# Performance work log

Hardware: AMD Instinct MI355X
Metric: run time of the kernel (lower is better)

Reference implementation:

```python
import jax, jax.numpy as jnp
import numpy as np

D = 128        # node/time feature dim (n_node_features)
E = 20         # edge feature dim (hard-coded in TGS)
N = 4096       # number of source nodes
K = 10         # neighbors per node (hard-coded n_neighbors=10)
NUM_NODES = 100000
NUM_EDGES = 500000


def setup_inputs() -> dict:
    key = jax.random.key(0)
    ks = jax.random.split(key, 11)
    node_features = jax.random.normal(ks[0], (NUM_NODES, D), jnp.float32)
    edge_features = jax.random.normal(ks[1], (NUM_EDGES, E), jnp.float32)
    source_nodes = jax.random.randint(ks[2], (N,), 0, NUM_NODES)
    timestamps = jax.random.uniform(ks[3], (N,), jnp.float32) * 1000.0
    neighbors1 = jax.random.randint(ks[4], (N, K), 0, NUM_NODES)
    edge_idxs1 = jax.random.randint(ks[5], (N, K), 0, NUM_EDGES)
    edge_times1 = jax.random.uniform(ks[6], (N, K), jnp.float32) * 1000.0
    neighbors2 = jax.random.randint(ks[7], (N * K, K), 0, NUM_NODES)
    edge_idxs2 = jax.random.randint(ks[8], (N * K, K), 0, NUM_EDGES)
    edge_times2 = jax.random.uniform(ks[9], (N * K, K), jnp.float32) * 1000.0
    # TimeEncode params (TGN init: w = 1/10^linspace(0,9,D), b = 0)
    time_w = jnp.asarray(1.0 / 10.0 ** np.linspace(0, 9, D), jnp.float32)
    time_b = jnp.zeros((D,), jnp.float32)
    pk = jax.random.split(ks[10], 4)
    s1 = float(1.0 / np.sqrt(2 * D + E))
    lin1_w = jax.random.uniform(pk[0], (2, 2 * D + E, D), jnp.float32, -s1, s1)
    lin1_b = jax.random.uniform(pk[1], (2, D), jnp.float32, -s1, s1)
    s2 = float(1.0 / np.sqrt(3 * D))
    lin2_w = jax.random.uniform(pk[2], (2, 3 * D, D), jnp.float32, -s2, s2)
    lin2_b = jax.random.uniform(pk[3], (2, D), jnp.float32, -s2, s2)
    return dict(node_features=node_features, edge_features=edge_features,
                source_nodes=source_nodes, timestamps=timestamps,
                neighbors1=neighbors1, edge_idxs1=edge_idxs1, edge_times1=edge_times1,
                neighbors2=neighbors2, edge_idxs2=edge_idxs2, edge_times2=edge_times2,
                time_w=time_w, time_b=time_b,
                lin1_w=lin1_w, lin1_b=lin1_b, lin2_w=lin2_w, lin2_b=lin2_b)


def reference(node_features, edge_features, source_nodes, timestamps,
              neighbors1, edge_idxs1, edge_times1,
              neighbors2, edge_idxs2, edge_times2,
              time_w, time_b, lin1_w, lin1_b, lin2_w, lin2_b):
    def time_enc(t):
        # TGN TimeEncode: cos(t * w + b), broadcast over feature dim
        return jnp.cos(t[..., None] * time_w + time_b)

    def aggregate(layer, src_feat, src_time_emb, nbr_emb, edge_time_emb, edge_feat):
        # GraphSumEmbedding.aggregate
        nf = jnp.concatenate([nbr_emb, edge_time_emb, edge_feat], axis=-1)  # [n, K, 2D+E]
        h = nf @ lin1_w[layer] + lin1_b[layer]                              # [n, K, D]
        nbr_sum = jax.nn.relu(h.sum(axis=1))                                # [n, D]
        sf = jnp.concatenate([src_feat, src_time_emb, nbr_sum], axis=-1)   # [n, 3D]
        return sf @ lin2_w[layer] + lin2_b[layer]                           # [n, D]

    n, k = neighbors1.shape
    ts1 = jnp.repeat(timestamps, k)  # timestamps for the N*K first-hop neighbors

    # recursion level 1 (layer index 0): embed the N*K first-hop neighbors;
    # their neighbors' (level-0) embeddings are raw node features.
    emb1 = aggregate(
        0,
        node_features[neighbors1.reshape(-1)],          # [N*K, D]
        time_enc(jnp.zeros_like(ts1)),                  # [N*K, D]
        node_features[neighbors2],                      # [N*K, K, D]
        time_enc(ts1[:, None] - edge_times2),           # [N*K, K, D]
        edge_features[edge_idxs2])                      # [N*K, K, E]

    # recursion level 2 (layer index 1): embed the N source nodes
    emb2 = aggregate(
        1,
        node_features[source_nodes],                    # [N, D]
        time_enc(jnp.zeros_like(timestamps)),           # [N, D]
        emb1.reshape(n, k, -1),                         # [N, K, D]
        time_enc(timestamps[:, None] - edge_times1),    # [N, K, D]
        edge_features[edge_idxs1])                      # [N, K, E]
    return emb2
```

## Files before the change

kernel.cpp:

```cpp
#include <hip/hip_runtime.h>

#define TGS_D 128
#define TGS_E 20
#define TGS_K 10
#define TGS_F1 276
#define LDA1 296
#define LDA2 264
#define RPB 16

typedef _Float16 f16;
typedef _Float16 f16x4 __attribute__((ext_vector_type(4)));
typedef _Float16 f16x8 __attribute__((ext_vector_type(8)));
typedef float    f32x4 __attribute__((ext_vector_type(4)));

__global__ void tgs_pack_w1(const float* __restrict__ W1, f16x8* __restrict__ PW1) {
    const int b = blockIdx.x, lane = threadIdx.x;
    const int layer = b / 72, rem = b % 72, ntile = rem / 9, kk = rem % 9;
    const int colg = ntile * 16 + (lane & 15);
    const int kbase = kk * 32 + (lane >> 4) * 8;
    f16x8 v;
    #pragma unroll
    for (int j = 0; j < 8; ++j) {
        const int k = kbase + j;
        v[j] = (k < TGS_F1) ? (f16)W1[(layer * TGS_F1 + k) * TGS_D + colg] : (f16)0.f;
    }
    PW1[b * 64 + lane] = v;
}

__global__ void tgs_pack_w2(const float* __restrict__ W2, f16x8* __restrict__ PW2) {
    const int b = blockIdx.x, lane = threadIdx.x;
    const int layer = b / 64, rem = b % 64, ntile = rem / 8, kk = rem % 8;
    const int colg = ntile * 16 + (lane & 15);
    const int kbase = kk * 32 + (lane >> 4) * 8;
    f16x8 v;
    #pragma unroll
    for (int j = 0; j < 8; ++j) {
        const int k = kbase + j;
        const int w2row = (k < TGS_D) ? k : (k + TGS_D);
        v[j] = (f16)W2[(layer * 3 * TGS_D + w2row) * TGS_D + colg];
    }
    PW2[b * 64 + lane] = v;
}

__global__ __launch_bounds__(128)
void tgs_tvec_kernel(const float* __restrict__ tb, const float* __restrict__ W2,
                     const float* __restrict__ B2, float* __restrict__ tvec) {
    const int l = blockIdx.x, d = threadIdx.x;
    const float* w = W2 + (l * 3 * TGS_D + TGS_D) * TGS_D;
    float acc = B2[l * TGS_D + d];
    for (int j = 0; j < TGS_D; ++j)
        acc = fmaf(__cosf(tb[j]), w[j * TGS_D + d], acc);
    tvec[l * TGS_D + d] = acc;
}

template<int LEVEL>
__global__ __launch_bounds__(256, 6)
void tgs_agg_kernel(
    const float* __restrict__ NF, const float* __restrict__ EF,
    const int* __restrict__ src_ids, const float* __restrict__ ts_arr,
    const int* __restrict__ nbr_idx,
    const int* __restrict__ eidx, const float* __restrict__ etime,
    const float* __restrict__ emb_in,
    const float* __restrict__ tw, const float* __restrict__ tb,
    const f16x8* __restrict__ PW1, const float* __restrict__ B1,
    const f16x8* __restrict__ PW2, const float* __restrict__ tvec,
    float* __restrict__ out)
{
    __shared__ f16 snf[RPB][LDA1];
    __shared__ f16 sf2[RPB][LDA2];
    __shared__ int   s_nbr[RPB * TGS_K];
    __shared__ int   s_eid[RPB * TGS_K];
    __shared__ float s_et [RPB * TGS_K];
    __shared__ float s_ts [RPB];

    const int tid = threadIdx.x;
    const int base_row = blockIdx.x * RPB;

    if (tid < RPB * TGS_K) {
        if (LEVEL == 1) s_nbr[tid] = nbr_idx[base_row * TGS_K + tid];
        s_eid[tid] = eidx[base_row * TGS_K + tid];
        s_et [tid] = etime[base_row * TGS_K + tid];
    }
    if (tid < RPB)
        s_ts[tid] = (LEVEL == 1) ? ts_arr[(base_row + tid) / TGS_K] : ts_arr[base_row + tid];
    __syncthreads();

    {
        const int sub = tid & 31;
        const int rr  = tid >> 5;
        const float4 wv = ((const float4*)tw)[sub];
        const float4 bv = ((const float4*)tb)[sub];
        #pragma unroll
        for (int h = 0; h < 2; ++h) {
            const int r   = h * 8 + rr;
            const int row = base_row + r;

            float4 a = make_float4(0.f, 0.f, 0.f, 0.f);
            if (LEVEL == 1) {
                #pragma unroll
                for (int k = 0; k < TGS_K; ++k) {
                    const int nb = s_nbr[r * TGS_K + k];
                    const float4 v = ((const float4*)(NF + nb * TGS_D))[sub];
                    a.x += v.x; a.y += v.y; a.z += v.z; a.w += v.w;
                }
            } else {
                #pragma unroll
                for (int k = 0; k < TGS_K; ++k) {
                    const float4 v = ((const float4*)(emb_in + (row * TGS_K + k) * TGS_D))[sub];
                    a.x += v.x; a.y += v.y; a.z += v.z; a.w += v.w;
                }
            }
            *(f16x4*)&snf[r][sub * 4] = f16x4{(f16)a.x, (f16)a.y, (f16)a.z, (f16)a.w};

            const int sid = src_ids[row];
            const float4 s = ((const float4*)(NF + sid * TGS_D))[sub];
            *(f16x4*)&sf2[r][sub * 4] = f16x4{(f16)s.x, (f16)s.y, (f16)s.z, (f16)s.w};

            const float ts = s_ts[r];
            float4 st = make_float4(0.f, 0.f, 0.f, 0.f);
            #pragma unroll
            for (int k = 0; k < TGS_K; ++k) {
                const float dt = ts - s_et[r * TGS_K + k];
                st.x += __cosf(fmaf(dt, wv.x, bv.x));
                st.y += __cosf(fmaf(dt, wv.y, bv.y));
                st.z += __cosf(fmaf(dt, wv.z, bv.z));
                st.w += __cosf(fmaf(dt, wv.w, bv.w));
            }
            *(f16x4*)&snf[r][TGS_D + sub * 4] = f16x4{(f16)st.x, (f16)st.y, (f16)st.z, (f16)st.w};

            if (sub < TGS_E / 4) {
                float4 e = make_float4(0.f, 0.f, 0.f, 0.f);
                #pragma unroll
                for (int k = 0; k < TGS_K; ++k) {
                    const int eb = s_eid[r * TGS_K + k];
                    const float4 v = ((const float4*)(EF + eb * TGS_E))[sub];
                    e.x += v.x; e.y += v.y; e.z += v.z; e.w += v.w;
                }
                *(f16x4*)&snf[r][2 * TGS_D + sub * 4] = f16x4{(f16)e.x, (f16)e.y, (f16)e.z, (f16)e.w};
            } else if (sub < 8) {
                *(f16x4*)&snf[r][2 * TGS_D + sub * 4] =
                    f16x4{(f16)0.f, (f16)0.f, (f16)0.f, (f16)0.f};
            }
        }
    }
    __syncthreads();

    const int lane = tid & 63;
    const int w    = tid >> 6;
    const int ccol = lane & 15;
    const int row0 = (lane >> 4) * 4;

    {
        f32x4 acc0 = {0.f, 0.f, 0.f, 0.f}, acc1 = acc0;
        const f16* abase = &snf[lane & 15][(lane >> 4) * 8];
        const int t0 = 2 * w, t1 = 2 * w + 1;
        #pragma unroll
        for (int kk = 0; kk < 9; ++kk) {
            const f16x8 af = *(const f16x8*)(abase + kk * 32);
            const f16x8 b0 = PW1[(t0 * 9 + kk) * 64 + lane];
            const f16x8 b1 = PW1[(t1 * 9 + kk) * 64 + lane];
            acc0 = __builtin_amdgcn_mfma_f32_16x16x32_f16(af, b0, acc0, 0, 0, 0);
            acc1 = __builtin_amdgcn_mfma_f32_16x16x32_f16(af, b1, acc1, 0, 0, 0);
        }
        const float b1v0 = 10.f * B1[t0 * 16 + ccol];
        const float b1v1 = 10.f * B1[t1 * 16 + ccol];
        #pragma unroll
        for (int i = 0; i < 4; ++i) {
            sf2[row0 + i][TGS_D + t0 * 16 + ccol] = (f16)fmaxf(acc0[i] + b1v0, 0.f);
            sf2[row0 + i][TGS_D + t1 * 16 + ccol] = (f16)fmaxf(acc1[i] + b1v1, 0.f);
        }
    }
    __syncthreads();

    {
        f32x4 acc0 = {0.f, 0.f, 0.f, 0.f}, acc1 = acc0;
        const f16* abase = &sf2[lane & 15][(lane >> 4) * 8];
        const int t0 = 2 * w, t1 = 2 * w + 1;
        #pragma unroll
        for (int kk = 0; kk < 8; ++kk) {
            const f16x8 af = *(const f16x8*)(abase + kk * 32);
            const f16x8 b0 = PW2[(t0 * 8 + kk) * 64 + lane];
            const f16x8 b1 = PW2[(t1 * 8 + kk) * 64 + lane];
            acc0 = __builtin_amdgcn_mfma_f32_16x16x32_f16(af, b0, acc0, 0, 0, 0);
            acc1 = __builtin_amdgcn_mfma_f32_16x16x32_f16(af, b1, acc1, 0, 0, 0);
        }
        const float tv0 = tvec[t0 * 16 + ccol];
        const float tv1 = tvec[t1 * 16 + ccol];
        #pragma unroll
        for (int i = 0; i < 4; ++i) {
            out[(base_row + row0 + i) * TGS_D + t0 * 16 + ccol] = acc0[i] + tv0;
            out[(base_row + row0 + i) * TGS_D + t1 * 16 + ccol] = acc1[i] + tv1;
        }
    }
}

extern "C" void kernel_launch(void* const* d_in, const int* in_sizes, int n_in,
                              void* d_out, int out_size, void* d_ws, size_t ws_size,
                              hipStream_t stream) {
    const float* NF   = (const float*)d_in[0];
    const float* EF   = (const float*)d_in[1];
    const int*   SRC  = (const int*)  d_in[2];
    const float* TS   = (const float*)d_in[3];
    const int*   NBR1 = (const int*)  d_in[4];
    const int*   EI1  = (const int*)  d_in[5];
    const float* ET1  = (const float*)d_in[6];
    const int*   NBR2 = (const int*)  d_in[7];
    const int*   EI2  = (const int*)  d_in[8];
    const float* ET2  = (const float*)d_in[9];
    const float* TW   = (const float*)d_in[10];
    const float* TB   = (const float*)d_in[11];
    const float* W1   = (const float*)d_in[12];
    const float* B1   = (const float*)d_in[13];
    const float* W2   = (const float*)d_in[14];
    const float* B2   = (const float*)d_in[15];

    float* emb1 = (float*)d_ws;
    char*  wsb  = (char*)d_ws + 40960 * TGS_D * 4;
    f16x8* PW1  = (f16x8*)wsb;
    f16x8* PW2  = (f16x8*)(wsb + 147456);
    float* tvec = (float*)(wsb + 147456 + 131072);

    tgs_pack_w1<<<2 * 8 * 9, 64, 0, stream>>>(W1, PW1);
    tgs_pack_w2<<<2 * 8 * 8, 64, 0, stream>>>(W2, PW2);
    tgs_tvec_kernel<<<2, 128, 0, stream>>>(TB, W2, B2, tvec);

    const int n1 = 4096 * TGS_K;
    const int n2 = 4096;

    tgs_agg_kernel<1><<<n1 / RPB, 256, 0, stream>>>(
        NF, EF, NBR1, TS, NBR2, EI2, ET2, nullptr,
        TW, TB, PW1, B1, PW2, tvec, emb1);

    tgs_agg_kernel<2><<<n2 / RPB, 256, 0, stream>>>(
        NF, EF, SRC, TS, nullptr, EI1, ET1, emb1,
        TW, TB,
        PW1 + 8 * 9 * 64, B1 + TGS_D,
        PW2 + 8 * 8 * 64, tvec + TGS_D,
        (float*)d_out);
}
```

Before: 74.30 us.

## Pre-convert node feature table to fp16 to halve neighbor gather bytes

```diff
diff --git a/kernel.cpp b/kernel.cpp
--- a/kernel.cpp
+++ b/kernel.cpp
@@ -13,50 +13,63 @@
 typedef _Float16 f16x8 __attribute__((ext_vector_type(8)));
 typedef float    f32x4 __attribute__((ext_vector_type(4)));
 
-__global__ void tgs_pack_w1(const float* __restrict__ W1, f16x8* __restrict__ PW1) {
-    const int b = blockIdx.x, lane = threadIdx.x;
-    const int layer = b / 72, rem = b % 72, ntile = rem / 9, kk = rem % 9;
-    const int colg = ntile * 16 + (lane & 15);
-    const int kbase = kk * 32 + (lane >> 4) * 8;
-    f16x8 v;
-    #pragma unroll
-    for (int j = 0; j < 8; ++j) {
-        const int k = kbase + j;
-        v[j] = (k < TGS_F1) ? (f16)W1[(layer * TGS_F1 + k) * TGS_D + colg] : (f16)0.f;
-    }
-    PW1[b * 64 + lane] = v;
-}
-
-__global__ void tgs_pack_w2(const float* __restrict__ W2, f16x8* __restrict__ PW2) {
-    const int b = blockIdx.x, lane = threadIdx.x;
-    const int layer = b / 64, rem = b % 64, ntile = rem / 8, kk = rem % 8;
-    const int colg = ntile * 16 + (lane & 15);
-    const int kbase = kk * 32 + (lane >> 4) * 8;
-    f16x8 v;
-    #pragma unroll
-    for (int j = 0; j < 8; ++j) {
-        const int k = kbase + j;
-        const int w2row = (k < TGS_D) ? k : (k + TGS_D);
-        v[j] = (f16)W2[(layer * 3 * TGS_D + w2row) * TGS_D + colg];
-    }
-    PW2[b * 64 + lane] = v;
+__global__ __launch_bounds__(256)
+void tgs_nf16(const float* __restrict__ NF, f16* __restrict__ NF16) {
+    const int i = (blockIdx.x * 256 + threadIdx.x) * 8;
+    const float4 a = *(const float4*)(NF + i);
+    const float4 b = *(const float4*)(NF + i + 4);
+    *(f16x8*)(NF16 + i) = f16x8{(f16)a.x, (f16)a.y, (f16)a.z, (f16)a.w,
+                                (f16)b.x, (f16)b.y, (f16)b.z, (f16)b.w};
 }
 
 __global__ __launch_bounds__(128)
-void tgs_tvec_kernel(const float* __restrict__ tb, const float* __restrict__ W2,
-                     const float* __restrict__ B2, float* __restrict__ tvec) {
-    const int l = blockIdx.x, d = threadIdx.x;
-    const float* w = W2 + (l * 3 * TGS_D + TGS_D) * TGS_D;
-    float acc = B2[l * TGS_D + d];
-    for (int j = 0; j < TGS_D; ++j)
-        acc = fmaf(__cosf(tb[j]), w[j * TGS_D + d], acc);
-    tvec[l * TGS_D + d] = acc;
+void tgs_setup(const float* __restrict__ W1, const float* __restrict__ W2,
+               const float* __restrict__ tb, const float* __restrict__ B2,
+               f16x8* __restrict__ PW1, f16x8* __restrict__ PW2,
+               float* __restrict__ tvec) {
+    const int b = blockIdx.x, tid = threadIdx.x;
+    if (b < 144) {
+        if (tid < 64) {
+            const int layer = b / 72, rem = b % 72, ntile = rem / 9, kk = rem % 9;
+            const int colg = ntile * 16 + (tid & 15);
+            const int kbase = kk * 32 + (tid >> 4) * 8;
+            f16x8 v;
+            #pragma unroll
+            for (int j = 0; j < 8; ++j) {
+                const int k = kbase + j;
+                v[j] = (k < TGS_F1) ? (f16)W1[(layer * TGS_F1 + k) * TGS_D + colg] : (f16)0.f;
+            }
+            PW1[b * 64 + tid] = v;
+        }
+    } else if (b < 272) {
+        if (tid < 64) {
+            const int bb = b - 144;
+            const int layer = bb / 64, rem = bb % 64, ntile = rem / 8, kk = rem % 8;
+            const int colg = ntile * 16 + (tid & 15);
+            const int kbase = kk * 32 + (tid >> 4) * 8;
+            f16x8 v;
+            #pragma unroll
+            for (int j = 0; j < 8; ++j) {
+                const int k = kbase + j;
+                const int w2row = (k < TGS_D) ? k : (k + TGS_D);
+                v[j] = (f16)W2[(layer * 3 * TGS_D + w2row) * TGS_D + colg];
+            }
+            PW2[bb * 64 + tid] = v;
+        }
+    } else {
+        const int l = b - 272, d = tid;
+        const float* w = W2 + (l * 3 * TGS_D + TGS_D) * TGS_D;
+        float acc = B2[l * TGS_D + d];
+        for (int j = 0; j < TGS_D; ++j)
+            acc = fmaf(__cosf(tb[j]), w[j * TGS_D + d], acc);
+        tvec[l * TGS_D + d] = acc;
+    }
 }
 
 template<int LEVEL>
 __global__ __launch_bounds__(256, 6)
 void tgs_agg_kernel(
-    const float* __restrict__ NF, const float* __restrict__ EF,
+    const f16* __restrict__ NF16, const float* __restrict__ EF,
     const int* __restrict__ src_ids, const float* __restrict__ ts_arr,
     const int* __restrict__ nbr_idx,
     const int* __restrict__ eidx, const float* __restrict__ etime,
@@ -86,61 +99,72 @@
     __syncthreads();
 
     {
-        const int sub = tid & 31;
-        const int rr  = tid >> 5;
-        const float4 wv = ((const float4*)tw)[sub];
-        const float4 bv = ((const float4*)tb)[sub];
-        #pragma unroll
-        for (int h = 0; h < 2; ++h) {
-            const int r   = h * 8 + rr;
-            const int row = base_row + r;
-
-            float4 a = make_float4(0.f, 0.f, 0.f, 0.f);
-            if (LEVEL == 1) {
+        const int sub = tid & 15;
+        const int r   = tid >> 4;
+        const int row = base_row + r;
+
+        float a[8] = {0.f, 0.f, 0.f, 0.f, 0.f, 0.f, 0.f, 0.f};
+        if (LEVEL == 1) {
+            #pragma unroll
+            for (int k = 0; k < TGS_K; ++k) {
+                const int nb = s_nbr[r * TGS_K + k];
+                const f16x8 v = *(const f16x8*)(NF16 + nb * TGS_D + sub * 8);
                 #pragma unroll
-                for (int k = 0; k < TGS_K; ++k) {
-                    const int nb = s_nbr[r * TGS_K + k];
-                    const float4 v = ((const float4*)(NF + nb * TGS_D))[sub];
-                    a.x += v.x; a.y += v.y; a.z += v.z; a.w += v.w;
-                }
-            } else {
-                #pragma unroll
-                for (int k = 0; k < TGS_K; ++k) {
-                    const float4 v = ((const float4*)(emb_in + (row * TGS_K + k) * TGS_D))[sub];
-                    a.x += v.x; a.y += v.y; a.z += v.z; a.w += v.w;
-                }
-            }
-            *(f16x4*)&snf[r][sub * 4] = f16x4{(f16)a.x, (f16)a.y, (f16)a.z, (f16)a.w};
-
-            const int sid = src_ids[row];
-            const float4 s = ((const float4*)(NF + sid * TGS_D))[sub];
-            *(f16x4*)&sf2[r][sub * 4] = f16x4{(f16)s.x, (f16)s.y, (f16)s.z, (f16)s.w};
-
-            const float ts = s_ts[r];
-            float4 st = make_float4(0.f, 0.f, 0.f, 0.f);
+                for (int j = 0; j < 8; ++j) a[j] += (float)v[j];
+            }
+        } else {
             #pragma unroll
             for (int k = 0; k < TGS_K; ++k) {
-                const float dt = ts - s_et[r * TGS_K + k];
-                st.x += __cosf(fmaf(dt, wv.x, bv.x));
-                st.y += __cosf(fmaf(dt, wv.y, bv.y));
-                st.z += __cosf(fmaf(dt, wv.z, bv.z));
-                st.w += __cosf(fmaf(dt, wv.w, bv.w));
-            }
-            *(f16x4*)&snf[r][TGS_D + sub * 4] = f16x4{(f16)st.x, (f16)st.y, (f16)st.z, (f16)st.w};
-
-            if (sub < TGS_E / 4) {
-                float4 e = make_float4(0.f, 0.f, 0.f, 0.f);
-                #pragma unroll
-                for (int k = 0; k < TGS_K; ++k) {
-                    const int eb = s_eid[r * TGS_K + k];
-                    const float4 v = ((const float4*)(EF + eb * TGS_E))[sub];
-                    e.x += v.x; e.y += v.y; e.z += v.z; e.w += v.w;
-                }
-                *(f16x4*)&snf[r][2 * TGS_D + sub * 4] = f16x4{(f16)e.x, (f16)e.y, (f16)e.z, (f16)e.w};
-            } else if (sub < 8) {
-                *(f16x4*)&snf[r][2 * TGS_D + sub * 4] =
-                    f16x4{(f16)0.f, (f16)0.f, (f16)0.f, (f16)0.f};
-            }
+                const float* p = emb_in + (row * TGS_K + k) * TGS_D + sub * 8;
+                const float4 u0 = ((const float4*)p)[0];
+                const float4 u1 = ((const float4*)p)[1];
+                a[0] += u0.x; a[1] += u0.y; a[2] += u0.z; a[3] += u0.w;
+                a[4] += u1.x; a[5] += u1.y; a[6] += u1.z; a[7] += u1.w;
+            }
+        }
+        f16x8 av;
+        #pragma unroll
+        for (int j = 0; j < 8; ++j) av[j] = (f16)a[j];
+        *(f16x8*)&snf[r][sub * 8] = av;
+
+        const int sid = src_ids[row];
+        *(f16x8*)&sf2[r][sub * 8] = *(const f16x8*)(NF16 + sid * TGS_D + sub * 8);
+
+        const float4 w0 = ((const float4*)tw)[sub * 2];
+        const float4 w1 = ((const float4*)tw)[sub * 2 + 1];
+        const float4 b0 = ((const float4*)tb)[sub * 2];
+        const float4 b1 = ((const float4*)tb)[sub * 2 + 1];
+        const float ts = s_ts[r];
+        float st[8] = {0.f, 0.f, 0.f, 0.f, 0.f, 0.f, 0.f, 0.f};
+        #pragma unroll
+        for (int k = 0; k < TGS_K; ++k) {
+            const float dt = ts - s_et[r * TGS_K + k];
+            st[0] += __cosf(fmaf(dt, w0.x, b0.x));
+            st[1] += __cosf(fmaf(dt, w0.y, b0.y));
+            st[2] += __cosf(fmaf(dt, w0.z, b0.z));
+            st[3] += __cosf(fmaf(dt, w0.w, b0.w));
+            st[4] += __cosf(fmaf(dt, w1.x, b1.x));
+            st[5] += __cosf(fmaf(dt, w1.y, b1.y));
+            st[6] += __cosf(fmaf(dt, w1.z, b1.z));
+            st[7] += __cosf(fmaf(dt, w1.w, b1.w));
+        }
+        f16x8 sv;
+        #pragma unroll
+        for (int j = 0; j < 8; ++j) sv[j] = (f16)st[j];
+        *(f16x8*)&snf[r][TGS_D + sub * 8] = sv;
+
+        if (sub < 5) {
+            float4 e = make_float4(0.f, 0.f, 0.f, 0.f);
+            #pragma unroll
+            for (int k = 0; k < TGS_K; ++k) {
+                const int eb = s_eid[r * TGS_K + k];
+                const float4 v = ((const float4*)(EF + eb * TGS_E))[sub];
+                e.x += v.x; e.y += v.y; e.z += v.z; e.w += v.w;
+            }
+            *(f16x4*)&snf[r][2 * TGS_D + sub * 4] = f16x4{(f16)e.x, (f16)e.y, (f16)e.z, (f16)e.w};
+        } else if (sub < 8) {
+            *(f16x4*)&snf[r][2 * TGS_D + sub * 4] =
+                f16x4{(f16)0.f, (f16)0.f, (f16)0.f, (f16)0.f};
         }
     }
     __syncthreads();
@@ -152,7 +176,7 @@
 
     {
         f32x4 acc0 = {0.f, 0.f, 0.f, 0.f}, acc1 = acc0;
-        const f16* abase = &snf[lane & 15][(lane >> 4) * 8];
+        const f16* abase = &snf[ccol][(lane >> 4) * 8];
         const int t0 = 2 * w, t1 = 2 * w + 1;
         #pragma unroll
         for (int kk = 0; kk < 9; ++kk) {
@@ -174,7 +198,7 @@
 
     {
         f32x4 acc0 = {0.f, 0.f, 0.f, 0.f}, acc1 = acc0;
-        const f16* abase = &sf2[lane & 15][(lane >> 4) * 8];
+        const f16* abase = &sf2[ccol][(lane >> 4) * 8];
         const int t0 = 2 * w, t1 = 2 * w + 1;
         #pragma unroll
         for (int kk = 0; kk < 8; ++kk) {
@@ -215,24 +239,24 @@
     const float* B2   = (const float*)d_in[15];
 
     float* emb1 = (float*)d_ws;
-    char*  wsb  = (char*)d_ws + 40960 * TGS_D * 4;
+    f16*   NF16 = (f16*)((char*)d_ws + 20971520);
+    char*  wsb  = (char*)d_ws + 20971520 + 25600000;
     f16x8* PW1  = (f16x8*)wsb;
     f16x8* PW2  = (f16x8*)(wsb + 147456);
     float* tvec = (float*)(wsb + 147456 + 131072);
 
-    tgs_pack_w1<<<2 * 8 * 9, 64, 0, stream>>>(W1, PW1);
-    tgs_pack_w2<<<2 * 8 * 8, 64, 0, stream>>>(W2, PW2);
-    tgs_tvec_kernel<<<2, 128, 0, stream>>>(TB, W2, B2, tvec);
+    tgs_nf16 <<<6250, 256, 0, stream>>>(NF, NF16);
+    tgs_setup<<<274, 128, 0, stream>>>(W1, W2, TB, B2, PW1, PW2, tvec);
 
     const int n1 = 4096 * TGS_K;
     const int n2 = 4096;
 
     tgs_agg_kernel<1><<<n1 / RPB, 256, 0, stream>>>(
-        NF, EF, NBR1, TS, NBR2, EI2, ET2, nullptr,
+        NF16, EF, NBR1, TS, NBR2, EI2, ET2, nullptr,
         TW, TB, PW1, B1, PW2, tvec, emb1);
 
     tgs_agg_kernel<2><<<n2 / RPB, 256, 0, stream>>>(
-        NF, EF, SRC, TS, nullptr, EI1, ET1, emb1,
+        NF16, EF, SRC, TS, nullptr, EI1, ET1, emb1,
         TW, TB,
         PW1 + 8 * 9 * 64, B1 + TGS_D,
         PW2 + 8 * 8 * 64, tvec + TGS_D,
```

Result: slower. 80.15 us (+7.9%).
